# Optimization experiments

Measured on AMD Instinct MI355X. Metric: run time of the kernel, lower is better.

The kernel has to match this reference:

```python
import math
import jax, jax.numpy as jnp
import numpy as np

# irreps_in == irreps_out == 256x0e + 256x1o + 128x2e
# (start, end, mul, ir_dim) for each irrep block in the flat feature vector
SEGS = [(0, 256, 256, 1), (256, 1024, 256, 3), (1024, 1664, 128, 5)]
DIM = 1664
BATCH = 32768
NW = sum(m * m for _, _, m, _ in SEGS)  # 147456
NB = 256  # bias only on scalar (0e) output


def setup_inputs() -> dict:
    key = jax.random.key(0)
    k1, k2, k3 = jax.random.split(key, 3)
    ws = jax.random.normal(k1, (NW,), dtype=jnp.float32)
    bs = jax.random.normal(k2, (NB,), dtype=jnp.float32)
    x = jax.random.normal(k3, (BATCH, DIM), dtype=jnp.float32)
    return {"ws": ws, "bs": bs, "x": x}


def reference(ws, bs, x):
    # Block-diagonal equivariant linear. Each instruction:
    #   out[i_out] += einsum('uw,ui->wi', w, x_block) / sqrt(mul_in * fan_in)
    # Here in/out irreps match 1:1, so fan_in = 1 for every output.
    w_off = 0
    outs = []
    for (s, e, mul, d) in SEGS:
        w = ws[w_off:w_off + mul * mul].reshape(mul, mul)
        w_off += mul * mul
        xb = x[:, s:e].reshape(-1, mul, d)  # [B, u, i]
        o = jnp.einsum('uw,bui->bwi', w, xb) * (1.0 / math.sqrt(mul))
        outs.append(o.reshape(-1, mul * d))
    # bias on the scalar (0e) output block only
    outs[0] = outs[0] + bs
    return jnp.concatenate(outs, axis=-1)  # [B, 1664]
```

## Files before the change

kernel.cpp:

```cpp
#include <hip/hip_runtime.h>


typedef short short8 __attribute__((ext_vector_type(8)));
typedef float f32x4 __attribute__((ext_vector_type(4)));

#define DIMF 1664
#define KB 64
#define LDA 72

__device__ __forceinline__ unsigned short f2bf(float f) {
  unsigned int u = __float_as_uint(f);
  u += 0x7fffu + ((u >> 16) & 1u);
  return (unsigned short)(u >> 16);
}

__global__ __launch_bounds__(256) void prep_w(const float* __restrict__ ws,
                                              unsigned short* __restrict__ wf) {
  int t = blockIdx.x * blockDim.x + threadIdx.x;
  int MUL, woff, goff;
  float scale;
  if (t < 8192) {
    MUL = 256; woff = 0; goff = 0; scale = 0.0625f;
  } else if (t < 16384) {
    MUL = 256; woff = 65536; goff = 8192; scale = 0.0625f;
  } else if (t < 18432) {
    MUL = 128; woff = 131072; goff = 16384; scale = 0.088388347648318447f;
  } else {
    return;
  }
  int g = t - goff;
  int l = g & 63;
  int nks = MUL >> 5;
  int ks = (g >> 6) % nks;
  int nt = g / (64 * nks);
  int n = nt * 16 + (l & 15);
  int kb = ks * 32 + (l >> 4) * 8;
  short8 v;
#pragma unroll
  for (int j = 0; j < 8; ++j)
    v[j] = (short)f2bf(ws[woff + (size_t)(kb + j) * MUL + n] * scale);
  *reinterpret_cast<short8*>(wf + (size_t)t * 8) = v;
}

template <int MUL, int D, int BMB, bool BIAS>
__device__ __forceinline__ void gemm_seg(const float* __restrict__ x,
                                         const unsigned short* __restrict__ wf,
                                         const float* __restrict__ bs,
                                         float* __restrict__ out, int blk, int s,
                                         unsigned short* A_lds) {
  constexpr int MT = BMB * D;
  constexpr int NMT = MT / 16;
  constexpr int NTW = MUL / 64;
  constexpr int NKS = MUL / 32;
  constexpr int NCH = MUL / KB;
  constexpr int KBD = KB * D;

  const int tid = threadIdx.x;
  const int lane = tid & 63;
  const int wave = tid >> 6;
  const int l15 = lane & 15;
  const int lhi = lane >> 4;
  const int b0 = blk * BMB;

  f32x4 acc[NMT][NTW];
#pragma unroll
  for (int a = 0; a < NMT; ++a)
#pragma unroll
    for (int b = 0; b < NTW; ++b) acc[a][b] = (f32x4){0.f, 0.f, 0.f, 0.f};

  for (int ch = 0; ch < NCH; ++ch) {
    {
      int idx = tid;
#pragma unroll
      for (int it = 0; it < (BMB * KBD / 4) / 256; ++it, idx += 256) {
        int r = idx / (KBD / 4);
        int c4 = idx % (KBD / 4);
        f32x4 v = *reinterpret_cast<const f32x4*>(
            x + (size_t)(b0 + r) * DIMF + s + ch * KBD + c4 * 4);
#pragma unroll
        for (int j = 0; j < 4; ++j) {
          int col = c4 * 4 + j;
          int u = col / D;
          int i = col - u * D;
          A_lds[(r * D + i) * LDA + u] = f2bf(v[j]);
        }
      }
    }
    __syncthreads();
#pragma unroll
    for (int ks = 0; ks < KB / 32; ++ks) {
      short8 af[NMT];
#pragma unroll
      for (int mt = 0; mt < NMT; ++mt)
        af[mt] = *reinterpret_cast<const short8*>(
            &A_lds[(mt * 16 + l15) * LDA + ks * 32 + lhi * 8]);
      int ksg = ch * (KB / 32) + ks;
#pragma unroll
      for (int nt = 0; nt < NTW; ++nt) {
        int ntg = wave * NTW + nt;
        short8 bfr = *reinterpret_cast<const short8*>(
            wf + ((size_t)(ntg * NKS + ksg) * 64 + lane) * 8);
#pragma unroll
        for (int mt = 0; mt < NMT; ++mt)
          acc[mt][nt] =
              __builtin_amdgcn_mfma_f32_16x16x32_bf16(af[mt], bfr, acc[mt][nt], 0, 0, 0);
      }
    }
    __syncthreads();
  }

#pragma unroll
  for (int nt = 0; nt < NTW; ++nt) {
    int n = wave * (MUL / 4) + nt * 16 + l15;
    float bias = 0.f;
    if (BIAS) bias = bs[n];
#pragma unroll
    for (int mt = 0; mt < NMT; ++mt) {
#pragma unroll
      for (int q = 0; q < 4; ++q) {
        int m = mt * 16 + lhi * 4 + q;
        int b = m / D;
        int i = m - b * D;
        out[(size_t)(b0 + b) * DIMF + s + n * D + i] = acc[mt][nt][q] + bias;
      }
    }
  }
}

__global__ __launch_bounds__(256) void linear_main(const float* __restrict__ x,
                                                   const unsigned short* __restrict__ wf,
                                                   const float* __restrict__ bs,
                                                   float* __restrict__ out) {
  __shared__ unsigned short A_lds[80 * LDA];
  int blk = blockIdx.x;
  if (blk < 512) {
    gemm_seg<256, 1, 64, true>(x, wf, bs, out, blk, 0, A_lds);
  } else if (blk < 2560) {
    gemm_seg<256, 3, 16, false>(x, wf + 65536, bs, out, blk - 512, 256, A_lds);
  } else {
    gemm_seg<128, 5, 16, false>(x, wf + 131072, bs, out, blk - 2560, 1024, A_lds);
  }
}

extern "C" void kernel_launch(void* const* d_in, const int* in_sizes, int n_in,
                              void* d_out, int out_size, void* d_ws, size_t ws_size,
                              hipStream_t stream) {
  const float* ws = (const float*)d_in[0];
  const float* bs = (const float*)d_in[1];
  const float* x = (const float*)d_in[2];
  float* out = (float*)d_out;
  unsigned short* wf = (unsigned short*)d_ws;

  hipLaunchKernelGGL(prep_w, dim3(72), dim3(256), 0, stream, ws, wf);
  hipLaunchKernelGGL(linear_main, dim3(512 + 2048 + 2048), dim3(256), 0, stream, x, wf,
                     bs, out);
}
```

Before: 127.6 us.

## Stage full K panel in LDS once with vectorized packed bf16 writes

Replaces the chunked K loop (two barriers per 64-wide chunk) with a single load of the whole K extent of the A tile into LDS, followed by one barrier and an uninterrupted MFMA loop. Each thread now loads D float4 vectors and writes packed 4-element bf16 groups instead of scalar shorts, which cuts the number of LDS store instructions. The scalar segment's batch tile is halved to 32 rows to double its block count. The larger LDS footprint (about 25KB) may reduce occupancy, and with no double buffering, global load latency is not overlapped with compute inside a block.

```diff
diff --git a/kernel.cpp b/kernel.cpp
--- a/kernel.cpp
+++ b/kernel.cpp
@@ -2,11 +2,10 @@
 
 
 typedef short short8 __attribute__((ext_vector_type(8)));
+typedef short short4v __attribute__((ext_vector_type(4)));
 typedef float f32x4 __attribute__((ext_vector_type(4)));
 
 #define DIMF 1664
-#define KB 64
-#define LDA 72
 
 __device__ __forceinline__ unsigned short f2bf(float f) {
   unsigned int u = __float_as_uint(f);
@@ -48,12 +47,13 @@
                                          const float* __restrict__ bs,
                                          float* __restrict__ out, int blk, int s,
                                          unsigned short* A_lds) {
+  constexpr int LDA = MUL + 8;
   constexpr int MT = BMB * D;
   constexpr int NMT = MT / 16;
   constexpr int NTW = MUL / 64;
   constexpr int NKS = MUL / 32;
-  constexpr int NCH = MUL / KB;
-  constexpr int KBD = KB * D;
+  constexpr int QPR = MUL / 4;
+  constexpr int NQ = BMB * QPR / 256;
 
   const int tid = threadIdx.x;
   const int lane = tid & 63;
@@ -62,51 +62,53 @@
   const int lhi = lane >> 4;
   const int b0 = blk * BMB;
 
+  {
+    int g = tid;
+#pragma unroll
+    for (int it = 0; it < NQ; ++it, g += 256) {
+      int r = g / QPR;
+      int q = g - r * QPR;
+      const float* src = x + (size_t)(b0 + r) * DIMF + s + q * 4 * D;
+      f32x4 v[D];
+#pragma unroll
+      for (int jd = 0; jd < D; ++jd)
+        v[jd] = reinterpret_cast<const f32x4*>(src)[jd];
+#pragma unroll
+      for (int i = 0; i < D; ++i) {
+        short4v p;
+#pragma unroll
+        for (int up = 0; up < 4; ++up) {
+          int j = up * D + i;
+          p[up] = (short)f2bf(v[j >> 2][j & 3]);
+        }
+        *reinterpret_cast<short4v*>(&A_lds[(r * D + i) * LDA + q * 4]) = p;
+      }
+    }
+  }
+  __syncthreads();
+
   f32x4 acc[NMT][NTW];
 #pragma unroll
   for (int a = 0; a < NMT; ++a)
 #pragma unroll
     for (int b = 0; b < NTW; ++b) acc[a][b] = (f32x4){0.f, 0.f, 0.f, 0.f};
 
-  for (int ch = 0; ch < NCH; ++ch) {
-    {
-      int idx = tid;
+  for (int ks = 0; ks < NKS; ++ks) {
+    short8 af[NMT];
 #pragma unroll
-      for (int it = 0; it < (BMB * KBD / 4) / 256; ++it, idx += 256) {
-        int r = idx / (KBD / 4);
-        int c4 = idx % (KBD / 4);
-        f32x4 v = *reinterpret_cast<const f32x4*>(
-            x + (size_t)(b0 + r) * DIMF + s + ch * KBD + c4 * 4);
+    for (int mt = 0; mt < NMT; ++mt)
+      af[mt] = *reinterpret_cast<const short8*>(
+          &A_lds[(mt * 16 + l15) * LDA + ks * 32 + lhi * 8]);
 #pragma unroll
-        for (int j = 0; j < 4; ++j) {
-          int col = c4 * 4 + j;
-          int u = col / D;
-          int i = col - u * D;
-          A_lds[(r * D + i) * LDA + u] = f2bf(v[j]);
-        }
-      }
-    }
-    __syncthreads();
-#pragma unroll
-    for (int ks = 0; ks < KB / 32; ++ks) {
-      short8 af[NMT];
+    for (int nt = 0; nt < NTW; ++nt) {
+      int ntg = wave * NTW + nt;
+      short8 bfr = *reinterpret_cast<const short8*>(
+          wf + ((size_t)(ntg * NKS + ks) * 64 + lane) * 8);
 #pragma unroll
       for (int mt = 0; mt < NMT; ++mt)
-        af[mt] = *reinterpret_cast<const short8*>(
-            &A_lds[(mt * 16 + l15) * LDA + ks * 32 + lhi * 8]);
-      int ksg = ch * (KB / 32) + ks;
-#pragma unroll
-      for (int nt = 0; nt < NTW; ++nt) {
-        int ntg = wave * NTW + nt;
-        short8 bfr = *reinterpret_cast<const short8*>(
-            wf + ((size_t)(ntg * NKS + ksg) * 64 + lane) * 8);
-#pragma unroll
-        for (int mt = 0; mt < NMT; ++mt)
-          acc[mt][nt] =
-              __builtin_amdgcn_mfma_f32_16x16x32_bf16(af[mt], bfr, acc[mt][nt], 0, 0, 0);
-      }
+        acc[mt][nt] =
+            __builtin_amdgcn_mfma_f32_16x16x32_bf16(af[mt], bfr, acc[mt][nt], 0, 0, 0);
     }
-    __syncthreads();
   }
 
 #pragma unroll
@@ -131,14 +133,14 @@
                                                    const unsigned short* __restrict__ wf,
                                                    const float* __restrict__ bs,
                                                    float* __restrict__ out) {
-  __shared__ unsigned short A_lds[80 * LDA];
+  __shared__ unsigned short A_lds[48 * 264];
   int blk = blockIdx.x;
-  if (blk < 512) {
-    gemm_seg<256, 1, 64, true>(x, wf, bs, out, blk, 0, A_lds);
-  } else if (blk < 2560) {
-    gemm_seg<256, 3, 16, false>(x, wf + 65536, bs, out, blk - 512, 256, A_lds);
+  if (blk < 1024) {
+    gemm_seg<256, 1, 32, true>(x, wf, bs, out, blk, 0, A_lds);
+  } else if (blk < 3072) {
+    gemm_seg<256, 3, 16, false>(x, wf + 65536, bs, out, blk - 1024, 256, A_lds);
   } else {
-    gemm_seg<128, 5, 16, false>(x, wf + 131072, bs, out, blk - 2560, 1024, A_lds);
+    gemm_seg<128, 5, 16, false>(x, wf + 131072, bs, out, blk - 3072, 1024, A_lds);
   }
 }
 
@@ -152,6 +154,6 @@
   unsigned short* wf = (unsigned short*)d_ws;
 
   hipLaunchKernelGGL(prep_w, dim3(72), dim3(256), 0, stream, ws, wf);
-  hipLaunchKernelGGL(linear_main, dim3(512 + 2048 + 2048), dim3(256), 0, stream, x, wf,
-                     bs, out);
+  hipLaunchKernelGGL(linear_main, dim3(1024 + 2048 + 2048), dim3(256), 0, stream, x,
+                     wf, bs, out);
 }
```

Result: faster. 120.5 us (-5.6%).
